# Kernel optimization log

Hardware: AMD Instinct MI355X
Metric: run time of the kernel (lower is better)

## Reference

```python
import jax, jax.numpy as jnp
import numpy as np

B = 8192
N_INPUT = 64
N_OUTPUT = 128
N_HIDDEN = 32
N_TARGETS = 2
N_EXOGS = 3
N_SERIES = N_TARGETS + N_EXOGS  # 5


def _init_linear(k, fan_in, w_shape, b_shape):
    # torch nn.Linear default init: U(-1/sqrt(fan_in), 1/sqrt(fan_in))
    bound = 1.0 / np.sqrt(fan_in)
    kw, kb = jax.random.split(k)
    W = jax.random.uniform(kw, w_shape, jnp.float32, -bound, bound)
    b = jax.random.uniform(kb, b_shape, jnp.float32, -bound, bound)
    return W, b


def setup_inputs() -> dict:
    key = jax.random.key(0)
    ks = jax.random.split(key, 5)
    target = jax.random.normal(ks[0], (B, N_INPUT, N_TARGETS), jnp.float32)
    exog = jax.random.normal(ks[1], (B, N_INPUT + N_OUTPUT, N_EXOGS), jnp.float32)
    # linear1: (n_input*n_series) -> n_targets
    W1, b1 = _init_linear(ks[2], N_INPUT * N_SERIES, (N_TARGETS, N_INPUT * N_SERIES), (N_TARGETS,))
    # linear2: n_series separate (n_input -> n_hidden) linears, stacked
    W2, b2 = _init_linear(ks[3], N_INPUT, (N_SERIES, N_HIDDEN, N_INPUT), (N_SERIES, N_HIDDEN))
    # linear3: (n_hidden*n_series) -> n_targets
    W3, b3 = _init_linear(ks[4], N_HIDDEN * N_SERIES, (N_TARGETS, N_HIDDEN * N_SERIES), (N_TARGETS,))
    return dict(target=target, exog=exog, W1=W1, b1=b1, W2=W2, b2=b2, W3=W3, b3=b3)


def _single_predict(window, ex, W1, b1, W2, b2, W3, b3):
    # window: (B, n_input, n_targets), ex: (B, n_input, n_exogs)
    te = jnp.concatenate([window, ex], axis=2)  # (B, n_input, n_series)
    flat = te.reshape(te.shape[0], -1)          # time-major, series fastest (torch Flatten order)
    out1 = flat @ W1.T + b1                     # (B, n_targets)
    # per-series tiny linears batched via einsum: h[b,i,:] = W2[i] @ te[b,:,i]
    h = jnp.einsum('bti,iht->bih', te, W2) + b2  # (B, n_series, n_hidden)
    h = jax.nn.sigmoid(h).reshape(h.shape[0], -1)  # series-major concat order matches torch.cat
    out2 = h @ W3.T + b3                        # (B, n_targets)
    return out1 + out2 + window[:, -1, :]


def reference(target, exog, W1, b1, W2, b2, W3, b3):
    def step(window, i):
        ex = jax.lax.dynamic_slice_in_dim(exog, i, N_INPUT, axis=1)  # (B, n_input, n_exogs)
        pred = _single_predict(window, ex, W1, b1, W2, b2, W3, b3)   # (B, n_targets)
        window = jnp.concatenate([window[:, 1:, :], pred[:, None, :]], axis=1)
        return window, pred

    _, preds = jax.lax.scan(step, target, jnp.arange(N_OUTPUT))
    return jnp.transpose(preds, (1, 0, 2))  # (B, n_output, n_targets)
```

## Files before the change

### kernel.cpp

```cpp
#include <hip/hip_runtime.h>
#include <math.h>

#define NB 8192
#define NIN 64
#define NOUT 128
#define NHID 32
#define NEXO 3
#define EXROWS 192
#define NTGT 2

typedef float f32x2 __attribute__((ext_vector_type(2)));
typedef float f32x4 __attribute__((ext_vector_type(4)));
typedef int   i32x4 __attribute__((ext_vector_type(4)));
typedef short bf16x8 __attribute__((ext_vector_type(8)));

#define WS_W2A  0
#define WS_W2BH 12288
#define WS_W2BL 20480
#define WS_WP   28672

__device__ __forceinline__ float sigmoidf(float x) {
    return 1.0f / (1.0f + __expf(-x));
}

__device__ __forceinline__ unsigned short f2bf(float x) {
    unsigned int u = __float_as_uint(x);
    unsigned int r = u + 0x7fffu + ((u >> 16) & 1u);
    return (unsigned short)(r >> 16);
}
__device__ __forceinline__ float bf2f(unsigned short h) {
    return __uint_as_float((unsigned int)h << 16);
}

template<int CTRL>
__device__ __forceinline__ float dpp_add(float x) {
    int p = __builtin_amdgcn_update_dpp(0, __float_as_int(x), CTRL, 0xf, 0xf, true);
    return x + __int_as_float(p);
}

#if __has_builtin(__builtin_amdgcn_permlane16_swap)
__device__ __forceinline__ f32x2 xchg16(f32x2 v, int s) {
    auto rx = __builtin_amdgcn_permlane16_swap(__float_as_uint(v.x), __float_as_uint(v.x), false, false);
    auto ry = __builtin_amdgcn_permlane16_swap(__float_as_uint(v.y), __float_as_uint(v.y), false, false);
    f32x2 r;
    r.x = s ? __uint_as_float(rx[0]) : __uint_as_float(rx[1]);
    r.y = s ? __uint_as_float(ry[0]) : __uint_as_float(ry[1]);
    return r;
}
#else
__device__ __forceinline__ f32x2 xchg16(f32x2 v, int s) {
    (void)s;
    f32x2 r;
    r.x = __int_as_float(__builtin_amdgcn_ds_swizzle(__float_as_int(v.x), 0x401f));
    r.y = __int_as_float(__builtin_amdgcn_ds_swizzle(__float_as_int(v.y), 0x401f));
    return r;
}
#endif

__device__ __forceinline__ f32x2 fold32(f32x2 v, int s32) {
    auto rx = __builtin_amdgcn_permlane32_swap(__float_as_uint(v.x), __float_as_uint(v.x), false, false);
    auto ry = __builtin_amdgcn_permlane32_swap(__float_as_uint(v.y), __float_as_uint(v.y), false, false);
    f32x2 o;
    o.x = v.x + (s32 ? __uint_as_float(rx[0]) : __uint_as_float(rx[1]));
    o.y = v.y + (s32 ? __uint_as_float(ry[0]) : __uint_as_float(ry[1]));
    return o;
}

__global__ __launch_bounds__(256) void narx_prepack_kernel(
    const float* __restrict__ W1, const float* __restrict__ W2,
    const float* __restrict__ W3, const float* __restrict__ b2,
    unsigned char* __restrict__ ws)
{
    const int tid = threadIdx.x;
    unsigned short* w2a  = (unsigned short*)(ws + WS_W2A);
    unsigned short* w2bh = (unsigned short*)(ws + WS_W2BH);
    unsigned short* w2bl = (unsigned short*)(ws + WS_W2BL);
    float* wp = (float*)(ws + WS_WP);

    for (int idx = tid; idx < 6144; idx += 256) {
        int rem = idx;
        int j = rem & 7;  rem >>= 3;
        int lg = rem & 3; rem >>= 2;
        int col = rem & 15; rem >>= 4;
        int kt = rem & 1; rem >>= 1;
        int mt = rem & 1; rem >>= 1;
        int e = rem;
        int row = 64 + e * 32 + mt * 16 + col;
        int t = kt * 32 + lg * 8 + j;
        w2a[idx] = f2bf(W2[(size_t)row * NIN + t]);
    }
    for (int idx = tid; idx < 4096; idx += 256) {
        int rem = idx;
        int j = rem & 7;   rem >>= 3;
        int k0g = rem & 3; rem >>= 2;
        int m0 = rem & 15; rem >>= 4;
        int kt = rem & 1;  rem >>= 1;
        int mt = rem;
        int row = mt * 16 + m0;
        int t = kt * 32 + k0g * 8 + j;
        float x = W2[(size_t)row * NIN + t];
        unsigned short hi = f2bf(x);
        w2bh[idx] = hi;
        w2bl[idx] = f2bf(x - bf2f(hi));
    }
    for (int idx = tid; idx < 384; idx += 256) {
        int e = idx >> 7;
        int r = idx & 127;
        int t = r >> 1, o = r & 1;
        wp[idx] = W1[o * 320 + t * 5 + 2 + e];
    }
    if (tid < 192) wp[384 + tid] = W3[(tid / 96) * 160 + 64 + (tid % 96)];
    if (tid < 96)  wp[576 + tid] = b2[64 + tid];
}

__global__ __launch_bounds__(256, 4) void narx_exog_kernel(
    const float* __restrict__ exog,
    const float* __restrict__ b1, const float* __restrict__ b3,
    const unsigned char* __restrict__ ws,
    float* __restrict__ E)
{
    __shared__ __align__(16) float exs[NEXO][EXROWS];
    __shared__ __align__(16) unsigned short exrep[NEXO * 8][200];
    __shared__ __align__(16) float2 w1e2[NEXO][NIN];
    __shared__ __align__(16) float w3l[2][96];
    __shared__ __align__(16) float b2l[96];

    const unsigned short* w2a = (const unsigned short*)(ws + WS_W2A);
    const float* wp = (const float*)(ws + WS_WP);

    const int tid = threadIdx.x;
    const int b = blockIdx.x;
    const float* exb = exog + (size_t)b * (EXROWS * NEXO);

    for (int idx = tid; idx < EXROWS * NEXO; idx += 256) {
        int t = idx / 3;
        int e = idx - t * 3;
        exs[e][t] = exb[idx];
    }
    for (int idx = tid; idx < 384; idx += 256) ((float*)w1e2)[idx] = wp[idx];
    if (tid < 192) ((float*)w3l)[tid] = wp[384 + tid];
    if (tid < 96)  b2l[tid] = wp[576 + tid];
    __syncthreads();

    for (int idx = tid; idx < NEXO * 8 * 192; idx += 256) {
        int e = idx / 1536;
        int rem = idx - e * 1536;
        int r = rem / 192;
        int q = rem - r * 192;
        float v = (q + r < 192) ? exs[e][q + r] : 0.f;
        exrep[e * 8 + r][q] = f2bf(v);
    }
    __syncthreads();

    const int wv = tid >> 6;
    const int l  = tid & 63;
    const int iw = wv * 32;
    const int lg = l >> 4;
    const int col = l & 15;

    float acc0[2] = {0.f, 0.f};
    float acc1[2] = {0.f, 0.f};

    #pragma unroll 1
    for (int e = 0; e < NEXO; ++e) {
        f32x4 b2v[2], w30v[2], w31v[2];
        #pragma unroll
        for (int mt = 0; mt < 2; ++mt) {
            b2v[mt]  = *(const f32x4*)&b2l[e * 32 + mt * 16 + lg * 4];
            w30v[mt] = *(const f32x4*)&w3l[0][e * 32 + mt * 16 + lg * 4];
            w31v[mt] = *(const f32x4*)&w3l[1][e * 32 + mt * 16 + lg * 4];
        }

        f32x4 cacc[2][2];
        #pragma unroll
        for (int mt = 0; mt < 2; ++mt)
            #pragma unroll
            for (int nt = 0; nt < 2; ++nt)
                cacc[mt][nt] = b2v[mt];

        #pragma unroll
        for (int kt = 0; kt < 2; ++kt) {
            bf16x8 af[2], bfr[2];
            #pragma unroll
            for (int mt = 0; mt < 2; ++mt)
                af[mt] = *(const bf16x8*)(w2a + ((size_t)((e * 2 + mt) * 2 + kt)) * 512
                                              + col * 32 + lg * 8);
            #pragma unroll
            for (int nt = 0; nt < 2; ++nt)
                bfr[nt] = *(const bf16x8*)&exrep[e * 8 + (l & 7)]
                              [iw + nt * 16 + kt * 32 + lg * 8 + ((l >> 3) & 1) * 8];
            #pragma unroll
            for (int mt = 0; mt < 2; ++mt)
                #pragma unroll
                for (int nt = 0; nt < 2; ++nt)
                    cacc[mt][nt] = __builtin_amdgcn_mfma_f32_16x16x32_bf16(
                        af[mt], bfr[nt], cacc[mt][nt], 0, 0, 0);
        }

        #pragma unroll
        for (int mt = 0; mt < 2; ++mt)
            #pragma unroll
            for (int nt = 0; nt < 2; ++nt) {
                #pragma unroll
                for (int r = 0; r < 4; ++r) {
                    float sg = sigmoidf(cacc[mt][nt][r]);
                    acc0[nt] += w30v[mt][r] * sg;
                    acc1[nt] += w31v[mt][r] * sg;
                }
            }

        const float* exs_e = &exs[e][0];
        #pragma unroll
        for (int dt = 0; dt < 16; ++dt) {
            float2 wv2 = w1e2[e][lg * 16 + dt];
            float x0 = exs_e[iw + l + dt];
            float x1 = exs_e[iw + 16 + l + dt];
            acc0[0] += wv2.x * x0;
            acc1[0] += wv2.y * x0;
            acc0[1] += wv2.x * x1;
            acc1[1] += wv2.y * x1;
        }
    }

    #pragma unroll
    for (int nt = 0; nt < 2; ++nt) {
        acc0[nt] += __shfl_xor(acc0[nt], 16, 64);
        acc0[nt] += __shfl_xor(acc0[nt], 32, 64);
        acc1[nt] += __shfl_xor(acc1[nt], 16, 64);
        acc1[nt] += __shfl_xor(acc1[nt], 32, 64);
    }
    if (lg == 0) {
        const float bias0 = b1[0] + b3[0];
        const float bias1 = b1[1] + b3[1];
        #pragma unroll
        for (int nt = 0; nt < 2; ++nt) {
            int i = iw + nt * 16 + col;
            *(float2*)&E[(size_t)b * (NOUT * NTGT) + i * 2] =
                make_float2(acc0[nt] + bias0, acc1[nt] + bias1);
        }
    }
}

#define CH 8
#define NCH 16

__global__ __launch_bounds__(64) void narx_recur_kernel(
    const float* __restrict__ target,
    const float* __restrict__ W1,
    const float* __restrict__ W2, const float* __restrict__ b2,
    const float* __restrict__ W3,
    const unsigned char* __restrict__ ws,
    float* __restrict__ out)
{
    __shared__ __align__(16) f32x2 yw[NTGT][EXROWS];
    __shared__ __align__(16) unsigned int ypk[NTGT][2][200];
    __shared__ __align__(16) f32x2 ew[NTGT][NOUT];
    __shared__ __align__(16) float pt[64][20];

    const unsigned short* w2bh = (const unsigned short*)(ws + WS_W2BH);
    const unsigned short* w2bl = (const unsigned short*)(ws + WS_W2BL);

    const int l = threadIdx.x;
    const int s   = (l >> 4) & 1;
    const int h   = (l & 15) | ((l >> 5) << 4);
    const int u   = s * NHID + h;
    const int s32 = (l >> 5) & 1;
    const size_t bA = (size_t)blockIdx.x * 2;
    const size_t bB = bA + 1;

    for (int i = l; i < NTGT * 2 * 200; i += 64) ((unsigned int*)ypk)[i] = 0u;

    {
        float4 eA = *(const float4*)&out[bA * (NOUT * NTGT) + l * 4];
        float4 eB = *(const float4*)&out[bB * (NOUT * NTGT) + l * 4];
        ew[0][2 * l]     = f32x2{eA.x, eB.x};
        ew[1][2 * l]     = f32x2{eA.y, eB.y};
        ew[0][2 * l + 1] = f32x2{eA.z, eB.z};
        ew[1][2 * l + 1] = f32x2{eA.w, eB.w};
    }
    {
        float2 tA = *(const float2*)&target[bA * (NIN * NTGT) + l * 2];
        float2 tB = *(const float2*)&target[bB * (NIN * NTGT) + l * 2];
        yw[0][l] = f32x2{tA.x, tB.x};
        yw[1][l] = f32x2{tA.y, tB.y};
        float v[2][2] = {{tA.x, tB.x}, {tA.y, tB.y}};
        #pragma unroll
        for (int ss = 0; ss < 2; ++ss)
            #pragma unroll
            for (int q = 0; q < 2; ++q) {
                unsigned short hi = f2bf(v[ss][q]);
                unsigned short lo = f2bf(v[ss][q] - bf2f(hi));
                ypk[ss][q][l] = (unsigned int)hi | ((unsigned int)lo << 16);
            }
    }

    bf16x8 ahf[4][2], alf[4][2];
    {
        const int m0 = l & 15, k0g = l >> 4;
        #pragma unroll
        for (int mt = 0; mt < 4; ++mt)
            #pragma unroll
            for (int kt = 0; kt < 2; ++kt) {
                const int off = ((mt * 2 + kt) * 16 + m0) * 32 + k0g * 8;
                ahf[mt][kt] = *(const bf16x8*)(w2bh + off);
                alf[mt][kt] = *(const bf16x8*)(w2bl + off);
            }
    }

    const float bb    = b2[u];
    const float w3own = W3[s * 160 + u];
    const float w3oth = W3[(1 - s) * 160 + u];
    const float wo1a  = W1[s * 320 + (2 * h) * 5 + s];
    const float wo1b  = W1[s * 320 + (2 * h + 1) * 5 + s];
    const float wo2a  = W1[(1 - s) * 320 + (2 * h) * 5 + s];
    const float wo2b  = W1[(1 - s) * 320 + (2 * h + 1) * 5 + s];
    float w2x[15];
    #pragma unroll
    for (int j = 0; j < 15; ++j) w2x[j] = W2[(size_t)u * NIN + 49 + j];

    f32x2* Y = &yw[s][0];
    const f32x2* EV = &ew[s][0];

    const int lag = l & 7;
    const int qb  = (l >> 3) & 1;
    const int bk0 = (l >> 4) * 8;
    const unsigned int* pk0 = &ypk[0][qb][0];
    const unsigned int* pk1 = &ypk[1][qb][0];

    auto mfma_to_pt = [&](const int i0m) {
        f32x4 acc[4];
        #pragma unroll
        for (int mt = 0; mt < 4; ++mt) acc[mt] = f32x4{0.f, 0.f, 0.f, 0.f};
        #pragma unroll
        for (int kt = 0; kt < 2; ++kt) {
            const int base = i0m + lag + bk0 + kt * 32;
            unsigned int r0[8], r1[8];
            #pragma unroll
            for (int j = 0; j < 8; ++j) { r0[j] = pk0[base + j]; r1[j] = pk1[base + j]; }
            i32x4 h0v, l0v, h1v, l1v;
            #pragma unroll
            for (int j2 = 0; j2 < 4; ++j2) {
                h0v[j2] = (int)__builtin_amdgcn_perm(r0[2*j2+1], r0[2*j2], 0x05040100u);
                l0v[j2] = (int)__builtin_amdgcn_perm(r0[2*j2+1], r0[2*j2], 0x07060302u);
                h1v[j2] = (int)__builtin_amdgcn_perm(r1[2*j2+1], r1[2*j2], 0x05040100u);
                l1v[j2] = (int)__builtin_amdgcn_perm(r1[2*j2+1], r1[2*j2], 0x07060302u);
            }
            const bf16x8 bh0 = __builtin_bit_cast(bf16x8, h0v);
            const bf16x8 bl0 = __builtin_bit_cast(bf16x8, l0v);
            const bf16x8 bh1 = __builtin_bit_cast(bf16x8, h1v);
            const bf16x8 bl1 = __builtin_bit_cast(bf16x8, l1v);
            #pragma unroll
            for (int mt = 0; mt < 4; ++mt) {
                const bf16x8 bh = (mt < 2) ? bh0 : bh1;
                const bf16x8 bl = (mt < 2) ? bl0 : bl1;
                acc[mt] = __builtin_amdgcn_mfma_f32_16x16x32_bf16(ahf[mt][kt], bh, acc[mt], 0, 0, 0);
                acc[mt] = __builtin_amdgcn_mfma_f32_16x16x32_bf16(ahf[mt][kt], bl, acc[mt], 0, 0, 0);
                acc[mt] = __builtin_amdgcn_mfma_f32_16x16x32_bf16(alf[mt][kt], bh, acc[mt], 0, 0, 0);
            }
        }
        const int n = l & 15, r0w = (l >> 4) * 4;
        #pragma unroll
        for (int mt = 0; mt < 4; ++mt)
            #pragma unroll
            for (int r = 0; r < 4; ++r)
                pt[mt * 16 + r0w + r][n] = acc[mt][r];
    };

    f32x2 P2[CH], corr[CH];
    mfma_to_pt(0);
    {
        f32x4 pa = *(const f32x4*)&pt[u][0];
        f32x4 pb = *(const f32x4*)&pt[u][4];
        f32x4 pc = *(const f32x4*)&pt[u][8];
        f32x4 pd = *(const f32x4*)&pt[u][12];
        #pragma unroll
        for (int ci = 0; ci < 4; ++ci) {
            P2[ci]     = f32x2{pa[ci], pc[ci]} + bb;
            P2[ci + 4] = f32x2{pb[ci], pd[ci]} + bb;
        }
    }
    #pragma unroll
    for (int j = 0; j < CH; ++j) corr[j] = f32x2{0.f, 0.f};

    #pragma unroll 1
    for (int c = 0; c < NCH; ++c) {
        const int i0 = c * CH;

        if (c > 0 && l < 16) {
            const int ss = l >> 3, j = l & 7;
            const int row = i0 + 56 + j;
            f32x2 v = yw[ss][row];
            unsigned short hA = f2bf(v.x);
            unsigned short hB = f2bf(v.y);
            ypk[ss][0][row] = (unsigned int)hA | ((unsigned int)f2bf(v.x - bf2f(hA)) << 16);
            ypk[ss][1][row] = (unsigned int)hB | ((unsigned int)f2bf(v.y - bf2f(hB)) << 16);
        }

        if (c + 1 < NCH) mfma_to_pt(i0 + CH);

        f32x2 ev8[CH];
        #pragma unroll
        for (int q = 0; q < 4; ++q) {
            f32x4 e4 = *(const f32x4*)&EV[i0 + 2 * q];
            ev8[2 * q]     = f32x2{e4[0], e4[1]};
            ev8[2 * q + 1] = f32x2{e4[2], e4[3]};
        }
        f32x2 predprev = Y[i0 + 63];

        #pragma unroll
        for (int ci = 0; ci < CH; ++ci) {
            const int i = i0 + ci;
            const f32x2 y1a = Y[i + 2 * h];
            const f32x2 y1b = Y[i + 2 * h + 1];

            f32x2 sg;
            sg.x = sigmoidf(P2[ci].x);
            sg.y = sigmoidf(P2[ci].y);

            f32x2 va = w3own * sg + wo1a * y1a + wo1b * y1b;
            f32x2 vb = w3oth * sg + wo2a * y1a + wo2b * y1b;

            f32x2 cc = va + xchg16(vb, s);
            cc.x = dpp_add<0xB1>(cc.x);  cc.y = dpp_add<0xB1>(cc.y);
            cc.x = dpp_add<0x4E>(cc.x);  cc.y = dpp_add<0x4E>(cc.y);
            cc.x = dpp_add<0x141>(cc.x); cc.y = dpp_add<0x141>(cc.y);
            cc.x = dpp_add<0x128>(cc.x); cc.y = dpp_add<0x128>(cc.y);
            cc = fold32(cc, s32);

            const f32x2 pred = cc + ev8[ci] + predprev;

            #pragma unroll
            for (int cj = ci + 1; cj < CH; ++cj)
                P2[cj] += w2x[15 - (cj - ci)] * pred;
            #pragma unroll
            for (int cin = 0; cin < CH; ++cin)
                corr[cin] += w2x[7 + ci - cin] * pred;

            if ((l & 47) == 0) Y[i + NIN] = pred;
            predprev = pred;
        }

        if (c + 1 < NCH) {
            f32x4 pa = *(const f32x4*)&pt[u][0];
            f32x4 pb = *(const f32x4*)&pt[u][4];
            f32x4 pc = *(const f32x4*)&pt[u][8];
            f32x4 pd = *(const f32x4*)&pt[u][12];
            #pragma unroll
            for (int ci = 0; ci < 4; ++ci) {
                P2[ci]     = f32x2{pa[ci], pc[ci]} + bb + corr[ci];
                P2[ci + 4] = f32x2{pb[ci], pd[ci]} + bb + corr[ci + 4];
            }
            #pragma unroll
            for (int j = 0; j < CH; ++j) corr[j] = f32x2{0.f, 0.f};
        }
    }

    {
        f32x2 a0 = yw[0][NIN + 2 * l];
        f32x2 a1 = yw[1][NIN + 2 * l];
        f32x2 c0 = yw[0][NIN + 2 * l + 1];
        f32x2 c1 = yw[1][NIN + 2 * l + 1];
        *(float4*)&out[bA * (NOUT * NTGT) + l * 4] = make_float4(a0.x, a1.x, c0.x, c1.x);
        *(float4*)&out[bB * (NOUT * NTGT) + l * 4] = make_float4(a0.y, a1.y, c0.y, c1.y);
    }
}

extern "C" void kernel_launch(void* const* d_in, const int* in_sizes, int n_in,
                              void* d_out, int out_size, void* d_ws, size_t ws_size,
                              hipStream_t stream) {
    (void)in_sizes; (void)n_in; (void)out_size; (void)ws_size;
    const float* target = (const float*)d_in[0];
    const float* exog   = (const float*)d_in[1];
    const float* W1     = (const float*)d_in[2];
    const float* b1     = (const float*)d_in[3];
    const float* W2     = (const float*)d_in[4];
    const float* b2     = (const float*)d_in[5];
    const float* W3     = (const float*)d_in[6];
    const float* b3     = (const float*)d_in[7];
    float* out = (float*)d_out;
    unsigned char* ws = (unsigned char*)d_ws;

    hipLaunchKernelGGL(narx_prepack_kernel, dim3(1), dim3(256), 0, stream,
                       W1, W2, W3, b2, ws);
    hipLaunchKernelGGL(narx_exog_kernel, dim3(NB), dim3(256), 0, stream,
                       exog, b1, b3, ws, out);
    hipLaunchKernelGGL(narx_recur_kernel, dim3(NB / 2), dim3(64), 0, stream,
                       target, W1, W2, b2, W3, ws, out);
}
```

Measured before the change: 203.3 us.

## Process one batch row per wave with 16-step chunks and drop MFMA lookahead

The recurrence kernel changes from two batch rows per 64-lane wave (packed as float2) to one row per wave, launching twice as many workgroups. The chunk size grows from 8 to 16 steps so each MFMA call covers 16 future steps. This removes the overlap of the next chunk's MFMA with the current scalar loop and the corr correction terms. W2 bf16 fragments are now reloaded from global memory every chunk instead of being held in registers, with an opaque zero offset that keeps the loads inside the loop. The aim is lower register pressure and more waves in flight, at the cost of the serial dependency chain being exposed and the work per row duplicated.

```diff
diff --git a/kernel.cpp b/kernel.cpp
--- a/kernel.cpp
+++ b/kernel.cpp
@@ -39,31 +39,20 @@
 }
 
 #if __has_builtin(__builtin_amdgcn_permlane16_swap)
-__device__ __forceinline__ f32x2 xchg16(f32x2 v, int s) {
-    auto rx = __builtin_amdgcn_permlane16_swap(__float_as_uint(v.x), __float_as_uint(v.x), false, false);
-    auto ry = __builtin_amdgcn_permlane16_swap(__float_as_uint(v.y), __float_as_uint(v.y), false, false);
-    f32x2 r;
-    r.x = s ? __uint_as_float(rx[0]) : __uint_as_float(rx[1]);
-    r.y = s ? __uint_as_float(ry[0]) : __uint_as_float(ry[1]);
-    return r;
+__device__ __forceinline__ float xchg16(float v, int s) {
+    auto rx = __builtin_amdgcn_permlane16_swap(__float_as_uint(v), __float_as_uint(v), false, false);
+    return s ? __uint_as_float(rx[0]) : __uint_as_float(rx[1]);
 }
 #else
-__device__ __forceinline__ f32x2 xchg16(f32x2 v, int s) {
+__device__ __forceinline__ float xchg16(float v, int s) {
     (void)s;
-    f32x2 r;
-    r.x = __int_as_float(__builtin_amdgcn_ds_swizzle(__float_as_int(v.x), 0x401f));
-    r.y = __int_as_float(__builtin_amdgcn_ds_swizzle(__float_as_int(v.y), 0x401f));
-    return r;
+    return __int_as_float(__builtin_amdgcn_ds_swizzle(__float_as_int(v), 0x401f));
 }
 #endif
 
-__device__ __forceinline__ f32x2 fold32(f32x2 v, int s32) {
-    auto rx = __builtin_amdgcn_permlane32_swap(__float_as_uint(v.x), __float_as_uint(v.x), false, false);
-    auto ry = __builtin_amdgcn_permlane32_swap(__float_as_uint(v.y), __float_as_uint(v.y), false, false);
-    f32x2 o;
-    o.x = v.x + (s32 ? __uint_as_float(rx[0]) : __uint_as_float(rx[1]));
-    o.y = v.y + (s32 ? __uint_as_float(ry[0]) : __uint_as_float(ry[1]));
-    return o;
+__device__ __forceinline__ float fold32(float v, int s32) {
+    auto rx = __builtin_amdgcn_permlane32_swap(__float_as_uint(v), __float_as_uint(v), false, false);
+    return v + (s32 ? __uint_as_float(rx[0]) : __uint_as_float(rx[1]));
 }
 
 __global__ __launch_bounds__(256) void narx_prepack_kernel(
@@ -241,8 +230,8 @@
     }
 }
 
-#define CH 8
-#define NCH 16
+#define CH 16
+#define NCH 8
 
 __global__ __launch_bounds__(64) void narx_recur_kernel(
     const float* __restrict__ target,
@@ -252,10 +241,10 @@
     const unsigned char* __restrict__ ws,
     float* __restrict__ out)
 {
-    __shared__ __align__(16) f32x2 yw[NTGT][EXROWS];
-    __shared__ __align__(16) unsigned int ypk[NTGT][2][200];
-    __shared__ __align__(16) f32x2 ew[NTGT][NOUT];
-    __shared__ __align__(16) float pt[64][20];
+    __shared__ __align__(16) float yw[NTGT][192];
+    __shared__ __align__(16) unsigned int ypk[NTGT][200];
+    __shared__ __align__(16) float ew[NTGT][NOUT];
+    __shared__ __align__(16) float pt[64][17];
 
     const unsigned short* w2bh = (const unsigned short*)(ws + WS_W2BH);
     const unsigned short* w2bl = (const unsigned short*)(ws + WS_W2BL);
@@ -265,46 +254,28 @@
     const int h   = (l & 15) | ((l >> 5) << 4);
     const int u   = s * NHID + h;
     const int s32 = (l >> 5) & 1;
-    const size_t bA = (size_t)blockIdx.x * 2;
-    const size_t bB = bA + 1;
-
-    for (int i = l; i < NTGT * 2 * 200; i += 64) ((unsigned int*)ypk)[i] = 0u;
+    const size_t b = blockIdx.x;
+
+    for (int i = l; i < NTGT * 200; i += 64) ((unsigned int*)ypk)[i] = 0u;
 
     {
-        float4 eA = *(const float4*)&out[bA * (NOUT * NTGT) + l * 4];
-        float4 eB = *(const float4*)&out[bB * (NOUT * NTGT) + l * 4];
-        ew[0][2 * l]     = f32x2{eA.x, eB.x};
-        ew[1][2 * l]     = f32x2{eA.y, eB.y};
-        ew[0][2 * l + 1] = f32x2{eA.z, eB.z};
-        ew[1][2 * l + 1] = f32x2{eA.w, eB.w};
+        float4 e4 = *(const float4*)&out[b * (NOUT * NTGT) + l * 4];
+        ew[0][2 * l]     = e4.x;
+        ew[1][2 * l]     = e4.y;
+        ew[0][2 * l + 1] = e4.z;
+        ew[1][2 * l + 1] = e4.w;
     }
     {
-        float2 tA = *(const float2*)&target[bA * (NIN * NTGT) + l * 2];
-        float2 tB = *(const float2*)&target[bB * (NIN * NTGT) + l * 2];
-        yw[0][l] = f32x2{tA.x, tB.x};
-        yw[1][l] = f32x2{tA.y, tB.y};
-        float v[2][2] = {{tA.x, tB.x}, {tA.y, tB.y}};
-        #pragma unroll
-        for (int ss = 0; ss < 2; ++ss)
-            #pragma unroll
-            for (int q = 0; q < 2; ++q) {
-                unsigned short hi = f2bf(v[ss][q]);
-                unsigned short lo = f2bf(v[ss][q] - bf2f(hi));
-                ypk[ss][q][l] = (unsigned int)hi | ((unsigned int)lo << 16);
-            }
-    }
-
-    bf16x8 ahf[4][2], alf[4][2];
-    {
-        const int m0 = l & 15, k0g = l >> 4;
-        #pragma unroll
-        for (int mt = 0; mt < 4; ++mt)
-            #pragma unroll
-            for (int kt = 0; kt < 2; ++kt) {
-                const int off = ((mt * 2 + kt) * 16 + m0) * 32 + k0g * 8;
-                ahf[mt][kt] = *(const bf16x8*)(w2bh + off);
-                alf[mt][kt] = *(const bf16x8*)(w2bl + off);
-            }
+        float2 tv = *(const float2*)&target[b * (NIN * NTGT) + l * 2];
+        yw[0][l] = tv.x;
+        yw[1][l] = tv.y;
+        float v[2] = {tv.x, tv.y};
+        #pragma unroll
+        for (int ss = 0; ss < 2; ++ss) {
+            unsigned short hi = f2bf(v[ss]);
+            unsigned short lo = f2bf(v[ss] - bf2f(hi));
+            ypk[ss][l] = (unsigned int)hi | ((unsigned int)lo << 16);
+        }
     }
 
     const float bb    = b2[u];
@@ -318,25 +289,38 @@
     #pragma unroll
     for (int j = 0; j < 15; ++j) w2x[j] = W2[(size_t)u * NIN + 49 + j];
 
-    f32x2* Y = &yw[s][0];
-    const f32x2* EV = &ew[s][0];
-
-    const int lag = l & 7;
-    const int qb  = (l >> 3) & 1;
+    float* Y = &yw[s][0];
+    const float* EV = &ew[s][0];
+
+    const int lag = l & 15;
     const int bk0 = (l >> 4) * 8;
-    const unsigned int* pk0 = &ypk[0][qb][0];
-    const unsigned int* pk1 = &ypk[1][qb][0];
-
-    auto mfma_to_pt = [&](const int i0m) {
+    const int m0 = l & 15, k0g = l >> 4;
+
+    int zoff = 0;
+
+    #pragma unroll 1
+    for (int c = 0; c < NCH; ++c) {
+        const int i0 = c * CH;
+        asm volatile("" : "+v"(zoff));
+
+        if (c > 0 && l < 32) {
+            const int ss = l >> 4, j = l & 15;
+            const int row = i0 + 48 + j;
+            float v = yw[ss][row];
+            unsigned short hi = f2bf(v);
+            ypk[ss][row] = (unsigned int)hi | ((unsigned int)f2bf(v - bf2f(hi)) << 16);
+        }
+
         f32x4 acc[4];
         #pragma unroll
         for (int mt = 0; mt < 4; ++mt) acc[mt] = f32x4{0.f, 0.f, 0.f, 0.f};
+
         #pragma unroll
         for (int kt = 0; kt < 2; ++kt) {
-            const int base = i0m + lag + bk0 + kt * 32;
+            const int base = i0 + lag + bk0 + kt * 32;
             unsigned int r0[8], r1[8];
             #pragma unroll
-            for (int j = 0; j < 8; ++j) { r0[j] = pk0[base + j]; r1[j] = pk1[base + j]; }
+            for (int j = 0; j < 8; ++j) { r0[j] = ypk[0][base + j]; r1[j] = ypk[1][base + j]; }
             i32x4 h0v, l0v, h1v, l1v;
             #pragma unroll
             for (int j2 = 0; j2 < 4; ++j2) {
@@ -351,117 +335,84 @@
             const bf16x8 bl1 = __builtin_bit_cast(bf16x8, l1v);
             #pragma unroll
             for (int mt = 0; mt < 4; ++mt) {
+                const int off = ((mt * 2 + kt) * 16 + m0) * 32 + k0g * 8 + zoff;
+                const bf16x8 ah = *(const bf16x8*)(w2bh + off);
+                const bf16x8 al = *(const bf16x8*)(w2bl + off);
                 const bf16x8 bh = (mt < 2) ? bh0 : bh1;
                 const bf16x8 bl = (mt < 2) ? bl0 : bl1;
-                acc[mt] = __builtin_amdgcn_mfma_f32_16x16x32_bf16(ahf[mt][kt], bh, acc[mt], 0, 0, 0);
-                acc[mt] = __builtin_amdgcn_mfma_f32_16x16x32_bf16(ahf[mt][kt], bl, acc[mt], 0, 0, 0);
-                acc[mt] = __builtin_amdgcn_mfma_f32_16x16x32_bf16(alf[mt][kt], bh, acc[mt], 0, 0, 0);
+                acc[mt] = __builtin_amdgcn_mfma_f32_16x16x32_bf16(ah, bh, acc[mt], 0, 0, 0);
+                acc[mt] = __builtin_amdgcn_mfma_f32_16x16x32_bf16(ah, bl, acc[mt], 0, 0, 0);
+                acc[mt] = __builtin_amdgcn_mfma_f32_16x16x32_bf16(al, bh, acc[mt], 0, 0, 0);
             }
         }
-        const int n = l & 15, r0w = (l >> 4) * 4;
-        #pragma unroll
-        for (int mt = 0; mt < 4; ++mt)
-            #pragma unroll
-            for (int r = 0; r < 4; ++r)
-                pt[mt * 16 + r0w + r][n] = acc[mt][r];
-    };
-
-    f32x2 P2[CH], corr[CH];
-    mfma_to_pt(0);
-    {
-        f32x4 pa = *(const f32x4*)&pt[u][0];
-        f32x4 pb = *(const f32x4*)&pt[u][4];
-        f32x4 pc = *(const f32x4*)&pt[u][8];
-        f32x4 pd = *(const f32x4*)&pt[u][12];
-        #pragma unroll
-        for (int ci = 0; ci < 4; ++ci) {
-            P2[ci]     = f32x2{pa[ci], pc[ci]} + bb;
-            P2[ci + 4] = f32x2{pb[ci], pd[ci]} + bb;
-        }
-    }
-    #pragma unroll
-    for (int j = 0; j < CH; ++j) corr[j] = f32x2{0.f, 0.f};
-
-    #pragma unroll 1
-    for (int c = 0; c < NCH; ++c) {
-        const int i0 = c * CH;
-
-        if (c > 0 && l < 16) {
-            const int ss = l >> 3, j = l & 7;
-            const int row = i0 + 56 + j;
-            f32x2 v = yw[ss][row];
-            unsigned short hA = f2bf(v.x);
-            unsigned short hB = f2bf(v.y);
-            ypk[ss][0][row] = (unsigned int)hA | ((unsigned int)f2bf(v.x - bf2f(hA)) << 16);
-            ypk[ss][1][row] = (unsigned int)hB | ((unsigned int)f2bf(v.y - bf2f(hB)) << 16);
-        }
-
-        if (c + 1 < NCH) mfma_to_pt(i0 + CH);
-
-        f32x2 ev8[CH];
-        #pragma unroll
-        for (int q = 0; q < 4; ++q) {
-            f32x4 e4 = *(const f32x4*)&EV[i0 + 2 * q];
-            ev8[2 * q]     = f32x2{e4[0], e4[1]};
-            ev8[2 * q + 1] = f32x2{e4[2], e4[3]};
-        }
-        f32x2 predprev = Y[i0 + 63];
-
-        #pragma unroll
-        for (int ci = 0; ci < CH; ++ci) {
-            const int i = i0 + ci;
-            const f32x2 y1a = Y[i + 2 * h];
-            const f32x2 y1b = Y[i + 2 * h + 1];
-
-            f32x2 sg;
-            sg.x = sigmoidf(P2[ci].x);
-            sg.y = sigmoidf(P2[ci].y);
-
-            f32x2 va = w3own * sg + wo1a * y1a + wo1b * y1b;
-            f32x2 vb = w3oth * sg + wo2a * y1a + wo2b * y1b;
-
-            f32x2 cc = va + xchg16(vb, s);
-            cc.x = dpp_add<0xB1>(cc.x);  cc.y = dpp_add<0xB1>(cc.y);
-            cc.x = dpp_add<0x4E>(cc.x);  cc.y = dpp_add<0x4E>(cc.y);
-            cc.x = dpp_add<0x141>(cc.x); cc.y = dpp_add<0x141>(cc.y);
-            cc.x = dpp_add<0x128>(cc.x); cc.y = dpp_add<0x128>(cc.y);
-            cc = fold32(cc, s32);
-
-            const f32x2 pred = cc + ev8[ci] + predprev;
-
-            #pragma unroll
-            for (int cj = ci + 1; cj < CH; ++cj)
-                P2[cj] += w2x[15 - (cj - ci)] * pred;
-            #pragma unroll
-            for (int cin = 0; cin < CH; ++cin)
-                corr[cin] += w2x[7 + ci - cin] * pred;
-
-            if ((l & 47) == 0) Y[i + NIN] = pred;
-            predprev = pred;
-        }
-
-        if (c + 1 < NCH) {
+
+        {
+            const int n = l & 15, r0w = (l >> 4) * 4;
+            #pragma unroll
+            for (int mt = 0; mt < 4; ++mt)
+                #pragma unroll
+                for (int r = 0; r < 4; ++r)
+                    pt[mt * 16 + r0w + r][n] = acc[mt][r];
+        }
+        float P2[CH];
+        {
             f32x4 pa = *(const f32x4*)&pt[u][0];
             f32x4 pb = *(const f32x4*)&pt[u][4];
             f32x4 pc = *(const f32x4*)&pt[u][8];
             f32x4 pd = *(const f32x4*)&pt[u][12];
             #pragma unroll
-            for (int ci = 0; ci < 4; ++ci) {
-                P2[ci]     = f32x2{pa[ci], pc[ci]} + bb + corr[ci];
-                P2[ci + 4] = f32x2{pb[ci], pd[ci]} + bb + corr[ci + 4];
+            for (int j = 0; j < 4; ++j) {
+                P2[j]      = pa[j] + bb;
+                P2[j + 4]  = pb[j] + bb;
+                P2[j + 8]  = pc[j] + bb;
+                P2[j + 12] = pd[j] + bb;
             }
-            #pragma unroll
-            for (int j = 0; j < CH; ++j) corr[j] = f32x2{0.f, 0.f};
+        }
+
+        float ev16[CH];
+        #pragma unroll
+        for (int q = 0; q < 4; ++q) {
+            f32x4 e4 = *(const f32x4*)&EV[i0 + 4 * q];
+            ev16[4*q+0] = e4[0]; ev16[4*q+1] = e4[1];
+            ev16[4*q+2] = e4[2]; ev16[4*q+3] = e4[3];
+        }
+        float predprev = Y[i0 + 63];
+
+        #pragma unroll
+        for (int ci = 0; ci < CH; ++ci) {
+            const int i = i0 + ci;
+            const float y1a = Y[i + 2 * h];
+            const float y1b = Y[i + 2 * h + 1];
+
+            const float sg = sigmoidf(P2[ci]);
+            float va = w3own * sg + wo1a * y1a + wo1b * y1b;
+            float vb = w3oth * sg + wo2a * y1a + wo2b * y1b;
+
+            float cc = va + xchg16(vb, s);
+            cc = dpp_add<0xB1>(cc);
+            cc = dpp_add<0x4E>(cc);
+            cc = dpp_add<0x141>(cc);
+            cc = dpp_add<0x128>(cc);
+            cc = fold32(cc, s32);
+
+            const float pred = cc + ev16[ci] + predprev;
+
+            #pragma unroll
+            for (int cj = ci + 1; cj < CH; ++cj)
+                P2[cj] += w2x[15 - (cj - ci)] * pred;
+
+            if ((l & 47) == 0) Y[i + NIN] = pred;
+            predprev = pred;
         }
     }
 
     {
-        f32x2 a0 = yw[0][NIN + 2 * l];
-        f32x2 a1 = yw[1][NIN + 2 * l];
-        f32x2 c0 = yw[0][NIN + 2 * l + 1];
-        f32x2 c1 = yw[1][NIN + 2 * l + 1];
-        *(float4*)&out[bA * (NOUT * NTGT) + l * 4] = make_float4(a0.x, a1.x, c0.x, c1.x);
-        *(float4*)&out[bB * (NOUT * NTGT) + l * 4] = make_float4(a0.y, a1.y, c0.y, c1.y);
+        float4 ov;
+        ov.x = yw[0][NIN + 2 * l];
+        ov.y = yw[1][NIN + 2 * l];
+        ov.z = yw[0][NIN + 2 * l + 1];
+        ov.w = yw[1][NIN + 2 * l + 1];
+        *(float4*)&out[b * (NOUT * NTGT) + l * 4] = ov;
     }
 }
 
@@ -484,6 +435,6 @@
                        W1, W2, W3, b2, ws);
     hipLaunchKernelGGL(narx_exog_kernel, dim3(NB), dim3(256), 0, stream,
                        exog, b1, b3, ws, out);
-    hipLaunchKernelGGL(narx_recur_kernel, dim3(NB / 2), dim3(64), 0, stream,
+    hipLaunchKernelGGL(narx_recur_kernel, dim3(NB), dim3(64), 0, stream,
                        target, W1, W2, b2, W3, ws, out);
 }
```

Result: faster. 197.5 us (-2.9%).
